# Performance work log

Measured on AMD Instinct MI355X. Metric: run time of the kernel, lower is better.

Reference implementation:

```python
import jax, jax.numpy as jnp
import numpy as np

B, T, DIM, H = 2, 2048, 512, 8
EPS = 1e-6


def setup_inputs() -> dict:
    key = jax.random.key(0)
    ks = jax.random.split(key, 6)
    scale = 0.05  # keep activations in a sane range for softmax/elu
    return {
        "x": jax.random.normal(ks[0], (B, T, DIM), dtype=jnp.float32),
        "Wq": jax.random.normal(ks[1], (DIM, DIM), dtype=jnp.float32) * scale,
        "Wk": jax.random.normal(ks[2], (DIM, DIM), dtype=jnp.float32) * scale,
        "Wv": jax.random.normal(ks[3], (DIM, DIM), dtype=jnp.float32) * scale,
        "Wo": jax.random.normal(ks[4], (DIM, DIM), dtype=jnp.float32) * scale,
        "bo": jax.random.normal(ks[5], (DIM,), dtype=jnp.float32) * scale,
    }


def reference(x, Wq, Wk, Wv, Wo, bo):
    b, t, dim = x.shape
    h = H
    d = dim // h
    # projections (nn.Linear: x @ W.T)
    q = x @ Wq.T
    k = x @ Wk.T
    v = x @ Wv.T
    mh = lambda z: z.reshape(b, t, h, d).transpose(0, 2, 1, 3)  # [b,h,t,d]
    q, k, v = mh(q), mh(k), mh(v)
    # causal linear attention with buckets = n (bucket size 1, no shift)
    q = jax.nn.softmax(q, axis=-1)
    k = jax.nn.elu(k) + 1.0  # psi
    k_cumsum = jnp.cumsum(k, axis=2)                       # [b,h,t,d]
    context = jnp.einsum('bhnd,bhne->bhnde', k, v)         # per-position outer products
    context = jnp.cumsum(context, axis=2)                  # causal prefix sum, [b,h,t,d,d]
    context = context / (k_cumsum[..., None] + EPS)        # safe_div
    attn = jnp.einsum('bhnd,bhnde->bhne', q, context)      # [b,h,t,d]
    out = attn.transpose(0, 2, 1, 3).reshape(b, t, dim)
    return out @ Wo.T + bo
```

## Files before the change

kernel.cpp:

```cpp
#include <hip/hip_runtime.h>

#define T_SEQ 2048
#define DIMM 512
#define NH 8
#define HD 64
#define BB 2
#define CHUNK 64
#define NCHUNK 32
#define EPSV 1e-6f
#define LDST 72
#define CST 132
#define PBUF 12288

typedef __attribute__((ext_vector_type(8))) short bf16x8;
typedef __attribute__((ext_vector_type(4))) short s16x4;
typedef __attribute__((ext_vector_type(4))) float f32x4;

static __device__ inline short f2bf(float f) {
    union { float f; unsigned u; } v; v.f = f;
    unsigned r = v.u + 0x7FFFu + ((v.u >> 16) & 1u);
    return (short)(r >> 16);
}
static __device__ inline float bf2f(short s) {
    union { unsigned u; float f; } v; v.u = ((unsigned)(unsigned short)s) << 16;
    return v.f;
}
static __device__ __forceinline__ void gload_lds16(const void* g, void* l) {
    __builtin_amdgcn_global_load_lds(
        (__attribute__((address_space(1))) void*)g,
        (__attribute__((address_space(3))) void*)l, 16, 0, 0);
}

__global__ __launch_bounds__(256) void convert_kernel(
    const float* __restrict__ x, const float* __restrict__ Wq,
    const float* __restrict__ Wk, const float* __restrict__ Wv,
    const float* __restrict__ Wo,
    short* __restrict__ xb, short* __restrict__ Wcat, short* __restrict__ Wob)
{
    const int u = blockIdx.x * 256 + threadIdx.x;
    const float* src; short* dst;
    if (u < 262144) {
        src = x + (size_t)u * 8; dst = xb + (size_t)u * 8;
    } else {
        const int v = u - 262144;
        const int o = (v & 32767) * 8;
        if (v < 32768)       { src = Wq + o; dst = Wcat + o; }
        else if (v < 65536)  { src = Wk + o; dst = Wcat + 262144 + o; }
        else if (v < 98304)  { src = Wv + o; dst = Wcat + 524288 + o; }
        else                 { src = Wo + o; dst = Wob + o; }
    }
    const float4 a = *(const float4*)src;
    const float4 b = *(const float4*)(src + 4);
    *(bf16x8*)dst = (bf16x8){f2bf(a.x), f2bf(a.y), f2bf(a.z), f2bf(a.w),
                             f2bf(b.x), f2bf(b.y), f2bf(b.z), f2bf(b.w)};
}

__global__ __launch_bounds__(256) void proj_mfma_kernel(
    const short* __restrict__ xb, const short* __restrict__ Wcat,
    short* __restrict__ Qs, short* __restrict__ Kbf,
    short* __restrict__ Ktb, short* __restrict__ Vt)
{
    __shared__ short S[2 * PBUF];
    short* Cs = S;
    const int m0 = blockIdx.x * 64;
    const int n0 = blockIdx.y * 128;
    const int which = blockIdx.y >> 2;
    const int tid = threadIdx.x;
    const int lane = tid & 63, w = tid >> 6;
    const int wr = w >> 1, wc = w & 1;
    const int fr = lane & 15, fg = lane >> 4;
    const int lrr = lane >> 3;
    const int sl8 = ((lane & 7) ^ lrr) * 8;
    const int xr = fr & 7;
    f32x4 acc[2][4] = {};

    #define STAGE(buf, k0)                                                       \
        {                                                                        \
            short* As_ = S + (buf) * PBUF;                                       \
            short* Bs_ = As_ + 4096;                                             \
            _Pragma("unroll")                                                    \
            for (int it = 0; it < 2; it++) {                                     \
                const int r0 = w * 16 + it * 8;                                  \
                gload_lds16(xb + (size_t)(m0 + r0 + lrr) * DIMM + (k0) + sl8,    \
                            &As_[r0 * 64]);                                      \
            }                                                                    \
            _Pragma("unroll")                                                    \
            for (int it = 0; it < 4; it++) {                                     \
                const int r0 = w * 32 + it * 8;                                  \
                gload_lds16(Wcat + (size_t)(n0 + r0 + lrr) * DIMM + (k0) + sl8,  \
                            &Bs_[r0 * 64]);                                      \
            }                                                                    \
        }

    STAGE(0, 0);
    STAGE(1, 64);

    #pragma unroll
    for (int t = 0; t < 8; t++) {
        if (t < 7) asm volatile("s_waitcnt vmcnt(6)" ::: "memory");
        else       asm volatile("s_waitcnt vmcnt(0)" ::: "memory");
        __builtin_amdgcn_sched_barrier(0);
        __builtin_amdgcn_s_barrier();
        __builtin_amdgcn_sched_barrier(0);
        {
            const short* As = S + (t & 1) * PBUF;
            const short* Bs = As + 4096;
            #pragma unroll
            for (int ks = 0; ks < 2; ks++) {
                const int cc = (((ks << 2) + fg) ^ xr) * 8;
                bf16x8 af[2], bfr[4];
                #pragma unroll
                for (int i = 0; i < 2; i++)
                    af[i] = *(const bf16x8*)&As[(wr * 32 + i * 16 + fr) * 64 + cc];
                #pragma unroll
                for (int j = 0; j < 4; j++)
                    bfr[j] = *(const bf16x8*)&Bs[(wc * 64 + j * 16 + fr) * 64 + cc];
                #pragma unroll
                for (int i = 0; i < 2; i++)
                    #pragma unroll
                    for (int j = 0; j < 4; j++)
                        acc[i][j] = __builtin_amdgcn_mfma_f32_16x16x32_bf16(af[i], bfr[j], acc[i][j], 0, 0, 0);
            }
        }
        __builtin_amdgcn_sched_barrier(0);
        __builtin_amdgcn_s_barrier();
        __builtin_amdgcn_sched_barrier(0);
        if (t < 6) STAGE(t & 1, (t + 2) * 64);
    }
    #undef STAGE

    #pragma unroll
    for (int i = 0; i < 2; i++)
        #pragma unroll
        for (int j = 0; j < 4; j++)
            #pragma unroll
            for (int reg = 0; reg < 4; reg++) {
                float val = acc[i][j][reg];
                if (which == 1) val = (val > 0.f) ? (val + 1.f) : __expf(val);
                Cs[(wr * 32 + i * 16 + fg * 4 + reg) * CST + wc * 64 + j * 16 + fr] = f2bf(val);
            }
    __syncthreads();

    const int b = m0 >> 11, t0 = m0 & (T_SEQ - 1);
    if (which == 0) {
        if (tid < 128) {
            const int r = tid & 63, hh = tid >> 6;
            const int head = (blockIdx.y & 3) * 2 + hh;
            s16x4 seg[16];
            #pragma unroll
            for (int s = 0; s < 16; s++) seg[s] = *(const s16x4*)&Cs[r * CST + hh * 64 + s * 4];
            float mx = -1e30f;
            #pragma unroll
            for (int s = 0; s < 16; s++)
                #pragma unroll
                for (int k = 0; k < 4; k++) mx = fmaxf(mx, bf2f(seg[s][k]));
            float sum = 0.f;
            #pragma unroll
            for (int s = 0; s < 16; s++)
                #pragma unroll
                for (int k = 0; k < 4; k++) sum += __expf(bf2f(seg[s][k]) - mx);
            const float inv = 1.f / sum;
            short* qp = Qs + (((size_t)(b * NH + head)) * T_SEQ + t0 + r) * HD;
            #pragma unroll
            for (int s = 0; s < 16; s += 2) {
                bf16x8 o;
                #pragma unroll
                for (int k = 0; k < 4; k++) o[k] = f2bf(__expf(bf2f(seg[s][k]) - mx) * inv);
                #pragma unroll
                for (int k = 0; k < 4; k++) o[4 + k] = f2bf(__expf(bf2f(seg[s + 1][k]) - mx) * inv);
                *(bf16x8*)(qp + s * 4) = o;
            }
        }
    } else if (which == 1) {
        if (tid < 128) {
            const int r = tid & 63, hh = tid >> 6;
            const int head = (blockIdx.y & 3) * 2 + hh;
            short* kp = Kbf + (((size_t)(b * NH + head)) * T_SEQ + t0 + r) * HD;
            #pragma unroll
            for (int s = 0; s < 8; s++) {
                const s16x4 a = *(const s16x4*)&Cs[r * CST + hh * 64 + s * 8];
                const s16x4 bq = *(const s16x4*)&Cs[r * CST + hh * 64 + s * 8 + 4];
                *(bf16x8*)(kp + s * 8) = (bf16x8){a[0], a[1], a[2], a[3], bq[0], bq[1], bq[2], bq[3]};
            }
        }
        {
            const int c = tid & 127, half = tid >> 7;
            const int head = (blockIdx.y & 3) * 2 + (c >> 6);
            const int d = c & 63;
            short* ktp = Ktb + (((size_t)(b * NH + head)) * HD + d) * T_SEQ + t0 + half * 32;
            #pragma unroll
            for (int s = 0; s < 4; s++) {
                bf16x8 o;
                #pragma unroll
                for (int k = 0; k < 8; k++) o[k] = Cs[(half * 32 + s * 8 + k) * CST + c];
                *(bf16x8*)(ktp + s * 8) = o;
            }
        }
    } else {
        const int c = tid & 127, half = tid >> 7;
        const int head = (blockIdx.y & 3) * 2 + (c >> 6);
        const int e = c & 63;
        short* vtp = Vt + (((size_t)(b * NH + head)) * HD + e) * T_SEQ + t0 + half * 32;
        #pragma unroll
        for (int s = 0; s < 4; s++) {
            bf16x8 o;
            #pragma unroll
            for (int k = 0; k < 8; k++) o[k] = Cs[(half * 32 + s * 8 + k) * CST + c];
            *(bf16x8*)(vtp + s * 8) = o;
        }
    }
}

__global__ __launch_bounds__(256) void chunk_sum_kernel(
    const short* __restrict__ Ktb, const short* __restrict__ Vt,
    float* __restrict__ Schunk, float* __restrict__ kchunk)
{
    __shared__ short VtL[64 * LDST];
    __shared__ short KtL[64 * LDST];
    __shared__ float ksp[4][64];
    const int bh = blockIdx.x >> 5, c = blockIdx.x & 31;
    const int tid = threadIdx.x;
    const int lane = tid & 63, w = tid >> 6;
    const int fr = lane & 15, fg = lane >> 4;
    #pragma unroll
    for (int it = 0; it < 2; it++) {
        const int qi = it * 256 + tid;
        const int r = qi >> 3, c8 = (qi & 7) * 8;
        *(bf16x8*)&VtL[r * LDST + c8] =
            *(const bf16x8*)(Vt + ((size_t)(bh * HD) + r) * T_SEQ + c * CHUNK + c8);
        *(bf16x8*)&KtL[r * LDST + c8] =
            *(const bf16x8*)(Ktb + ((size_t)(bh * HD) + r) * T_SEQ + c * CHUNK + c8);
    }
    __syncthreads();
    f32x4 acc[4] = {};
    #pragma unroll
    for (int ks = 0; ks < 2; ks++) {
        const bf16x8 av = *(const bf16x8*)&VtL[(w * 16 + fr) * LDST + ks * 32 + fg * 8];
        #pragma unroll
        for (int j = 0; j < 4; j++) {
            const bf16x8 bk = *(const bf16x8*)&KtL[(j * 16 + fr) * LDST + ks * 32 + fg * 8];
            acc[j] = __builtin_amdgcn_mfma_f32_16x16x32_bf16(av, bk, acc[j], 0, 0, 0);
        }
    }
    float* Sout = Schunk + ((size_t)bh * NCHUNK + c) * 4096;
    #pragma unroll
    for (int j = 0; j < 4; j++)
        #pragma unroll
        for (int reg = 0; reg < 4; reg++)
            Sout[(w * 16 + fg * 4 + reg) * 64 + j * 16 + fr] = acc[j][reg];
    float ps = 0.f;
    #pragma unroll
    for (int t = 0; t < 16; t++) ps += bf2f(KtL[lane * LDST + w * 16 + t]);
    ksp[w][lane] = ps;
    __syncthreads();
    if (tid < 64)
        kchunk[((size_t)bh * NCHUNK + c) * 64 + tid] =
            ksp[0][tid] + ksp[1][tid] + ksp[2][tid] + ksp[3][tid];
}

__global__ __launch_bounds__(256) void scan_kernel(float* __restrict__ Schunk,
                                                   float* __restrict__ kchunk)
{
    const int gid = blockIdx.x * 256 + threadIdx.x;
    if (blockIdx.x < 256) {
        const int bh = gid >> 12, i = gid & 4095;
        float run = 0.f;
        float* p = Schunk + (size_t)bh * NCHUNK * 4096 + i;
        for (int c = 0; c < NCHUNK; c++) { const float tv = p[c * 4096]; p[c * 4096] = run; run += tv; }
    } else {
        const int idx = gid - 65536;
        const int bh = idx >> 6, d = idx & 63;
        float run = 0.f;
        float* p = kchunk + (size_t)bh * NCHUNK * 64 + d;
        for (int c = 0; c < NCHUNK; c++) { const float tv = p[c * 64]; p[c * 64] = run; run += tv; }
    }
}

__global__ __launch_bounds__(256) void intra_kernel(
    const short* __restrict__ Qs, const short* __restrict__ Kbf,
    const short* __restrict__ Vt, const float* __restrict__ Schunk,
    const float* __restrict__ kchunk, short* __restrict__ attnb)
{
    __shared__ short B1[64 * LDST];
    __shared__ short B2[64 * LDST];
    __shared__ short KL[64 * LDST];
    __shared__ short VtL[64 * LDST];
    __shared__ short QnL[64 * LDST];
    __shared__ float gsum[4][64];
    __shared__ float kpre[64];
    const int bh = blockIdx.x >> 5, c = blockIdx.x & 31;
    const int tid = threadIdx.x;
    const int lane = tid & 63, w = tid >> 6;
    const int fr = lane & 15, fg = lane >> 4;
    const size_t tdbase = ((size_t)bh * T_SEQ + c * CHUNK) * HD;
    #pragma unroll
    for (int it = 0; it < 2; it++) {
        const int qi = it * 256 + tid;
        const int r = qi >> 3, c8 = (qi & 7) * 8;
        *(bf16x8*)&B1[r * LDST + c8]  = *(const bf16x8*)(Qs + tdbase + r * HD + c8);
        *(bf16x8*)&KL[r * LDST + c8]  = *(const bf16x8*)(Kbf + tdbase + r * HD + c8);
        *(bf16x8*)&VtL[r * LDST + c8] =
            *(const bf16x8*)(Vt + ((size_t)(bh * HD) + r) * T_SEQ + c * CHUNK + c8);
    }
    {
        const float* Sp = Schunk + ((size_t)bh * NCHUNK + c) * 4096;
        #pragma unroll
        for (int it = 0; it < 4; it++) {
            const int qi = it * 256 + tid;
            const int r = qi >> 4, c4 = (qi & 15) * 4;
            const float4 v = *(const float4*)(Sp + r * 64 + c4);
            *(s16x4*)&B2[r * LDST + c4] = (s16x4){f2bf(v.x), f2bf(v.y), f2bf(v.z), f2bf(v.w)};
        }
    }
    if (tid < 64) kpre[tid] = kchunk[((size_t)bh * NCHUNK + c) * 64 + tid];
    __syncthreads();
    {
        float s = 0.f;
        #pragma unroll
        for (int t = 0; t < 16; t++) s += bf2f(KL[(w * 16 + t) * LDST + lane]);
        gsum[w][lane] = s;
    }
    __syncthreads();
    {
        float run = kpre[lane];
        for (int gg = 0; gg < w; gg++) run += gsum[gg][lane];
        #pragma unroll
        for (int t0 = 0; t0 < 16; t0++) {
            const int t = w * 16 + t0;
            run += bf2f(KL[t * LDST + lane]);
            const float qv = bf2f(B1[t * LDST + lane]);
            QnL[t * LDST + lane] = f2bf(qv / (run + EPSV));
        }
    }
    __syncthreads();
    {
        f32x4 a1[4] = {};
        #pragma unroll
        for (int ks = 0; ks < 2; ks++) {
            const bf16x8 aq = *(const bf16x8*)&QnL[(w * 16 + fr) * LDST + ks * 32 + fg * 8];
            #pragma unroll
            for (int j = 0; j < 4; j++) {
                const bf16x8 bk = *(const bf16x8*)&KL[(j * 16 + fr) * LDST + ks * 32 + fg * 8];
                a1[j] = __builtin_amdgcn_mfma_f32_16x16x32_bf16(aq, bk, a1[j], 0, 0, 0);
            }
        }
        const int trow = w * 16 + fg * 4;
        #pragma unroll
        for (int j = 0; j < 4; j++)
            #pragma unroll
            for (int reg = 0; reg < 4; reg++) {
                const int t = trow + reg, s = j * 16 + fr;
                B1[t * LDST + s] = (s <= t) ? f2bf(a1[j][reg]) : (short)0;
            }
    }
    __syncthreads();
    {
        f32x4 a2[4] = {};
        #pragma unroll
        for (int ks = 0; ks < 2; ks++) {
            const bf16x8 aq = *(const bf16x8*)&QnL[(w * 16 + fr) * LDST + ks * 32 + fg * 8];
            const bf16x8 aa = *(const bf16x8*)&B1[(w * 16 + fr) * LDST + ks * 32 + fg * 8];
            #pragma unroll
            for (int j = 0; j < 4; j++) {
                const bf16x8 bs = *(const bf16x8*)&B2[(j * 16 + fr) * LDST + ks * 32 + fg * 8];
                const bf16x8 bv = *(const bf16x8*)&VtL[(j * 16 + fr) * LDST + ks * 32 + fg * 8];
                a2[j] = __builtin_amdgcn_mfma_f32_16x16x32_bf16(aq, bs, a2[j], 0, 0, 0);
                a2[j] = __builtin_amdgcn_mfma_f32_16x16x32_bf16(aa, bv, a2[j], 0, 0, 0);
            }
        }
        short* ap = attnb + tdbase;
        const int trow = w * 16 + fg * 4;
        #pragma unroll
        for (int j = 0; j < 4; j++)
            #pragma unroll
            for (int reg = 0; reg < 4; reg++)
                ap[(trow + reg) * HD + j * 16 + fr] = f2bf(a2[j][reg]);
    }
}

__global__ __launch_bounds__(256) void outproj_mfma_kernel(
    const short* __restrict__ attnb, const short* __restrict__ Wob,
    const float* __restrict__ bo, float* __restrict__ out)
{
    __shared__ short As[64 * 64];
    __shared__ short Bs[64 * 64];
    const int m0 = blockIdx.x * 64;
    const int n0 = blockIdx.y * 64;
    const int tid = threadIdx.x;
    const int lane = tid & 63, w = tid >> 6;
    const int fr = lane & 15, fg = lane >> 4;
    const int lr = lane >> 3, lc = (lane & 7) * 8;
    const int b = m0 >> 11, tbase = m0 & (T_SEQ - 1);
    f32x4 acc[4] = {};
    for (int k0 = 0; k0 < DIMM; k0 += 64) {
        const int h = k0 >> 6;
        #pragma unroll
        for (int it = 0; it < 2; it++) {
            const int r0 = w * 16 + it * 8;
            gload_lds16(attnb + (((size_t)(b * NH + h)) * T_SEQ + tbase + r0 + lr) * HD + lc,
                        &As[r0 * 64]);
            gload_lds16(Wob + (size_t)(n0 + r0 + lr) * DIMM + k0 + lc, &Bs[r0 * 64]);
        }
        __syncthreads();
        #pragma unroll
        for (int ks = 0; ks < 2; ks++) {
            const bf16x8 af = *(const bf16x8*)&As[(w * 16 + fr) * 64 + ks * 32 + fg * 8];
            #pragma unroll
            for (int j = 0; j < 4; j++) {
                const bf16x8 bfr = *(const bf16x8*)&Bs[(j * 16 + fr) * 64 + ks * 32 + fg * 8];
                acc[j] = __builtin_amdgcn_mfma_f32_16x16x32_bf16(af, bfr, acc[j], 0, 0, 0);
            }
        }
        __syncthreads();
    }
    #pragma unroll
    for (int j = 0; j < 4; j++)
        #pragma unroll
        for (int reg = 0; reg < 4; reg++) {
            const int m = m0 + w * 16 + fg * 4 + reg;
            const int n = n0 + j * 16 + fr;
            out[(size_t)m * DIMM + n] = acc[j][reg] + bo[n];
        }
}

extern "C" void kernel_launch(void* const* d_in, const int* in_sizes, int n_in,
                              void* d_out, int out_size, void* d_ws, size_t ws_size,
                              hipStream_t stream)
{
    const float* x  = (const float*)d_in[0];
    const float* Wq = (const float*)d_in[1];
    const float* Wk = (const float*)d_in[2];
    const float* Wv = (const float*)d_in[3];
    const float* Wo = (const float*)d_in[4];
    const float* bo = (const float*)d_in[5];
    float* out = (float*)d_out;

    const size_t NELEM = (size_t)BB * T_SEQ * DIMM;
    short* xb    = (short*)d_ws;
    short* Wcat  = xb + NELEM;
    short* Wob   = Wcat + 786432;
    short* Qs    = Wob + 262144;
    short* Kbf   = Qs + NELEM;
    short* Ktb   = Kbf + NELEM;
    short* Vt    = Ktb + NELEM;
    short* attnb = Vt + NELEM;
    float* Schunk = (float*)(attnb + NELEM);
    float* kchunk = Schunk + (size_t)BB * NH * NCHUNK * 4096;

    convert_kernel<<<dim3(1536), 256, 0, stream>>>(x, Wq, Wk, Wv, Wo, xb, Wcat, Wob);
    proj_mfma_kernel<<<dim3(64, 12), 256, 0, stream>>>(xb, Wcat, Qs, Kbf, Ktb, Vt);
    chunk_sum_kernel<<<dim3(BB * NH * NCHUNK), 256, 0, stream>>>(Ktb, Vt, Schunk, kchunk);
    scan_kernel<<<dim3(260), 256, 0, stream>>>(Schunk, kchunk);
    intra_kernel<<<dim3(BB * NH * NCHUNK), 256, 0, stream>>>(Qs, Kbf, Vt, Schunk, kchunk, attnb);
    outproj_mfma_kernel<<<dim3(64, 8), 256, 0, stream>>>(attnb, Wob, bo, out);
}
```

Baseline: 54.82 us.

## Widen projection GEMM tile to 64x256 per block with four heads

Measured after the change: 55.80 us. About the same (+1.8%).

```diff
diff --git a/kernel.cpp b/kernel.cpp
--- a/kernel.cpp
+++ b/kernel.cpp
@@ -9,8 +9,8 @@
 #define NCHUNK 32
 #define EPSV 1e-6f
 #define LDST 72
-#define CST 132
-#define PBUF 12288
+#define CSTW 258
+#define PB 20480
 
 typedef __attribute__((ext_vector_type(8))) short bf16x8;
 typedef __attribute__((ext_vector_type(4))) short s16x4;
@@ -60,23 +60,24 @@
     short* __restrict__ Qs, short* __restrict__ Kbf,
     short* __restrict__ Ktb, short* __restrict__ Vt)
 {
-    __shared__ short S[2 * PBUF];
+    extern __shared__ short S[];
     short* Cs = S;
     const int m0 = blockIdx.x * 64;
-    const int n0 = blockIdx.y * 128;
-    const int which = blockIdx.y >> 2;
+    const int n0 = blockIdx.y * 256;
+    const int which = blockIdx.y >> 1;
+    const int headbase = (blockIdx.y & 1) * 4;
     const int tid = threadIdx.x;
     const int lane = tid & 63, w = tid >> 6;
-    const int wr = w >> 1, wc = w & 1;
     const int fr = lane & 15, fg = lane >> 4;
     const int lrr = lane >> 3;
     const int sl8 = ((lane & 7) ^ lrr) * 8;
     const int xr = fr & 7;
-    f32x4 acc[2][4] = {};
+    const int b = m0 >> 11, t0 = m0 & (T_SEQ - 1);
+    f32x4 acc[4][4] = {};
 
     #define STAGE(buf, k0)                                                       \
         {                                                                        \
-            short* As_ = S + (buf) * PBUF;                                       \
+            short* As_ = S + (buf) * PB;                                         \
             short* Bs_ = As_ + 4096;                                             \
             _Pragma("unroll")                                                    \
             for (int it = 0; it < 2; it++) {                                     \
@@ -85,8 +86,8 @@
                             &As_[r0 * 64]);                                      \
             }                                                                    \
             _Pragma("unroll")                                                    \
-            for (int it = 0; it < 4; it++) {                                     \
-                const int r0 = w * 32 + it * 8;                                  \
+            for (int it = 0; it < 8; it++) {                                     \
+                const int r0 = w * 64 + it * 8;                                  \
                 gload_lds16(Wcat + (size_t)(n0 + r0 + lrr) * DIMM + (k0) + sl8,  \
                             &Bs_[r0 * 64]);                                      \
             }                                                                    \
@@ -97,29 +98,31 @@
 
     #pragma unroll
     for (int t = 0; t < 8; t++) {
-        if (t < 7) asm volatile("s_waitcnt vmcnt(6)" ::: "memory");
+        if (t < 7) asm volatile("s_waitcnt vmcnt(10)" ::: "memory");
         else       asm volatile("s_waitcnt vmcnt(0)" ::: "memory");
         __builtin_amdgcn_sched_barrier(0);
         __builtin_amdgcn_s_barrier();
         __builtin_amdgcn_sched_barrier(0);
         {
-            const short* As = S + (t & 1) * PBUF;
+            const short* As = S + (t & 1) * PB;
             const short* Bs = As + 4096;
             #pragma unroll
             for (int ks = 0; ks < 2; ks++) {
                 const int cc = (((ks << 2) + fg) ^ xr) * 8;
-                bf16x8 af[2], bfr[4];
+                bf16x8 af[4], bfr[4];
                 #pragma unroll
-                for (int i = 0; i < 2; i++)
-                    af[i] = *(const bf16x8*)&As[(wr * 32 + i * 16 + fr) * 64 + cc];
+                for (int i = 0; i < 4; i++)
+                    af[i] = *(const bf16x8*)&As[(i * 16 + fr) * 64 + cc];
                 #pragma unroll
                 for (int j = 0; j < 4; j++)
-                    bfr[j] = *(const bf16x8*)&Bs[(wc * 64 + j * 16 + fr) * 64 + cc];
+                    bfr[j] = *(const bf16x8*)&Bs[(w * 64 + j * 16 + fr) * 64 + cc];
+                __builtin_amdgcn_s_setprio(1);
                 #pragma unroll
-                for (int i = 0; i < 2; i++)
+                for (int i = 0; i < 4; i++)
                     #pragma unroll
                     for (int j = 0; j < 4; j++)
                         acc[i][j] = __builtin_amdgcn_mfma_f32_16x16x32_bf16(af[i], bfr[j], acc[i][j], 0, 0, 0);
+                __builtin_amdgcn_s_setprio(0);
             }
         }
         __builtin_amdgcn_sched_barrier(0);
@@ -130,82 +133,88 @@
     #undef STAGE
 
     #pragma unroll
-    for (int i = 0; i < 2; i++)
+    for (int i = 0; i < 4; i++)
         #pragma unroll
         for (int j = 0; j < 4; j++)
             #pragma unroll
             for (int reg = 0; reg < 4; reg++) {
                 float val = acc[i][j][reg];
                 if (which == 1) val = (val > 0.f) ? (val + 1.f) : __expf(val);
-                Cs[(wr * 32 + i * 16 + fg * 4 + reg) * CST + wc * 64 + j * 16 + fr] = f2bf(val);
-            }
-    __syncthreads();
-
-    const int b = m0 >> 11, t0 = m0 & (T_SEQ - 1);
+                Cs[(i * 16 + fg * 4 + reg) * CSTW + w * 64 + j * 16 + fr] = f2bf(val);
+            }
+    __syncthreads();
+
     if (which == 0) {
-        if (tid < 128) {
-            const int r = tid & 63, hh = tid >> 6;
-            const int head = (blockIdx.y & 3) * 2 + hh;
-            s16x4 seg[16];
-            #pragma unroll
-            for (int s = 0; s < 16; s++) seg[s] = *(const s16x4*)&Cs[r * CST + hh * 64 + s * 4];
-            float mx = -1e30f;
-            #pragma unroll
-            for (int s = 0; s < 16; s++)
-                #pragma unroll
-                for (int k = 0; k < 4; k++) mx = fmaxf(mx, bf2f(seg[s][k]));
-            float sum = 0.f;
-            #pragma unroll
-            for (int s = 0; s < 16; s++)
-                #pragma unroll
-                for (int k = 0; k < 4; k++) sum += __expf(bf2f(seg[s][k]) - mx);
-            const float inv = 1.f / sum;
-            short* qp = Qs + (((size_t)(b * NH + head)) * T_SEQ + t0 + r) * HD;
-            #pragma unroll
-            for (int s = 0; s < 16; s += 2) {
+        const int row = tid & 63, hl = tid >> 6;
+        const int head = headbase + hl;
+        const unsigned* cr = (const unsigned*)&Cs[row * CSTW + hl * 64];
+        unsigned u[32];
+        #pragma unroll
+        for (int s = 0; s < 32; s++) u[s] = cr[s];
+        float mx = -1e30f;
+        #pragma unroll
+        for (int s = 0; s < 32; s++) {
+            mx = fmaxf(mx, bf2f((short)(u[s] & 0xffff)));
+            mx = fmaxf(mx, bf2f((short)(u[s] >> 16)));
+        }
+        float sum = 0.f;
+        #pragma unroll
+        for (int s = 0; s < 32; s++) {
+            sum += __expf(bf2f((short)(u[s] & 0xffff)) - mx);
+            sum += __expf(bf2f((short)(u[s] >> 16)) - mx);
+        }
+        const float inv = 1.f / sum;
+        short* qp = Qs + (((size_t)(b * NH + head)) * T_SEQ + t0 + row) * HD;
+        #pragma unroll
+        for (int g = 0; g < 8; g++) {
+            bf16x8 o;
+            #pragma unroll
+            for (int k = 0; k < 4; k++) {
+                const unsigned uv = u[g * 4 + k];
+                o[2 * k]     = f2bf(__expf(bf2f((short)(uv & 0xffff)) - mx) * inv);
+                o[2 * k + 1] = f2bf(__expf(bf2f((short)(uv >> 16)) - mx) * inv);
+            }
+            *(bf16x8*)(qp + g * 8) = o;
+        }
+    } else if (which == 1) {
+        {
+            const int row = tid & 63, hl = tid >> 6;
+            const int head = headbase + hl;
+            const unsigned* cr = (const unsigned*)&Cs[row * CSTW + hl * 64];
+            short* kp = Kbf + (((size_t)(b * NH + head)) * T_SEQ + t0 + row) * HD;
+            #pragma unroll
+            for (int g = 0; g < 8; g++) {
                 bf16x8 o;
                 #pragma unroll
-                for (int k = 0; k < 4; k++) o[k] = f2bf(__expf(bf2f(seg[s][k]) - mx) * inv);
-                #pragma unroll
-                for (int k = 0; k < 4; k++) o[4 + k] = f2bf(__expf(bf2f(seg[s + 1][k]) - mx) * inv);
-                *(bf16x8*)(qp + s * 4) = o;
-            }
-        }
-    } else if (which == 1) {
-        if (tid < 128) {
-            const int r = tid & 63, hh = tid >> 6;
-            const int head = (blockIdx.y & 3) * 2 + hh;
-            short* kp = Kbf + (((size_t)(b * NH + head)) * T_SEQ + t0 + r) * HD;
+                for (int k = 0; k < 4; k++) {
+                    const unsigned uv = cr[g * 4 + k];
+                    o[2 * k]     = (short)(uv & 0xffff);
+                    o[2 * k + 1] = (short)(uv >> 16);
+                }
+                *(bf16x8*)(kp + g * 8) = o;
+            }
+        }
+        {
+            const int col = tid;
+            const int head = headbase + (col >> 6), d = col & 63;
+            short* ktp = Ktb + (((size_t)(b * NH + head)) * HD + d) * T_SEQ + t0;
             #pragma unroll
             for (int s = 0; s < 8; s++) {
-                const s16x4 a = *(const s16x4*)&Cs[r * CST + hh * 64 + s * 8];
-                const s16x4 bq = *(const s16x4*)&Cs[r * CST + hh * 64 + s * 8 + 4];
-                *(bf16x8*)(kp + s * 8) = (bf16x8){a[0], a[1], a[2], a[3], bq[0], bq[1], bq[2], bq[3]};
-            }
-        }
-        {
-            const int c = tid & 127, half = tid >> 7;
-            const int head = (blockIdx.y & 3) * 2 + (c >> 6);
-            const int d = c & 63;
-            short* ktp = Ktb + (((size_t)(b * NH + head)) * HD + d) * T_SEQ + t0 + half * 32;
-            #pragma unroll
-            for (int s = 0; s < 4; s++) {
                 bf16x8 o;
                 #pragma unroll
-                for (int k = 0; k < 8; k++) o[k] = Cs[(half * 32 + s * 8 + k) * CST + c];
+                for (int k = 0; k < 8; k++) o[k] = Cs[(s * 8 + k) * CSTW + col];
                 *(bf16x8*)(ktp + s * 8) = o;
             }
         }
     } else {
-        const int c = tid & 127, half = tid >> 7;
-        const int head = (blockIdx.y & 3) * 2 + (c >> 6);
-        const int e = c & 63;
-        short* vtp = Vt + (((size_t)(b * NH + head)) * HD + e) * T_SEQ + t0 + half * 32;
-        #pragma unroll
-        for (int s = 0; s < 4; s++) {
+        const int col = tid;
+        const int head = headbase + (col >> 6), e = col & 63;
+        short* vtp = Vt + (((size_t)(b * NH + head)) * HD + e) * T_SEQ + t0;
+        #pragma unroll
+        for (int s = 0; s < 8; s++) {
             bf16x8 o;
             #pragma unroll
-            for (int k = 0; k < 8; k++) o[k] = Cs[(half * 32 + s * 8 + k) * CST + c];
+            for (int k = 0; k < 8; k++) o[k] = Cs[(s * 8 + k) * CSTW + col];
             *(bf16x8*)(vtp + s * 8) = o;
         }
     }
@@ -447,8 +456,15 @@
     float* Schunk = (float*)(attnb + NELEM);
     float* kchunk = Schunk + (size_t)BB * NH * NCHUNK * 4096;
 
+    static bool attr_set = false;
+    if (!attr_set) {
+        hipFuncSetAttribute((const void*)proj_mfma_kernel,
+                            hipFuncAttributeMaxDynamicSharedMemorySize, 2 * PB * 2);
+        attr_set = true;
+    }
+
     convert_kernel<<<dim3(1536), 256, 0, stream>>>(x, Wq, Wk, Wv, Wo, xb, Wcat, Wob);
-    proj_mfma_kernel<<<dim3(64, 12), 256, 0, stream>>>(xb, Wcat, Qs, Kbf, Ktb, Vt);
+    proj_mfma_kernel<<<dim3(64, 6), 256, 2 * PB * 2, stream>>>(xb, Wcat, Qs, Kbf, Ktb, Vt);
     chunk_sum_kernel<<<dim3(BB * NH * NCHUNK), 256, 0, stream>>>(Ktb, Vt, Schunk, kchunk);
     scan_kernel<<<dim3(260), 256, 0, stream>>>(Schunk, kchunk);
     intra_kernel<<<dim3(BB * NH * NCHUNK), 256, 0, stream>>>(Qs, Kbf, Vt, Schunk, kchunk, attnb);
```

## Fold chunk-state prefix scan into intra kernel, drop separate scan launch

Applied to the files above, without the earlier changes.

Result: slower. 66.85 us (+21.9%).

```diff
diff --git a/kernel.cpp b/kernel.cpp
--- a/kernel.cpp
+++ b/kernel.cpp
@@ -258,24 +258,6 @@
             ksp[0][tid] + ksp[1][tid] + ksp[2][tid] + ksp[3][tid];
 }
 
-__global__ __launch_bounds__(256) void scan_kernel(float* __restrict__ Schunk,
-                                                   float* __restrict__ kchunk)
-{
-    const int gid = blockIdx.x * 256 + threadIdx.x;
-    if (blockIdx.x < 256) {
-        const int bh = gid >> 12, i = gid & 4095;
-        float run = 0.f;
-        float* p = Schunk + (size_t)bh * NCHUNK * 4096 + i;
-        for (int c = 0; c < NCHUNK; c++) { const float tv = p[c * 4096]; p[c * 4096] = run; run += tv; }
-    } else {
-        const int idx = gid - 65536;
-        const int bh = idx >> 6, d = idx & 63;
-        float run = 0.f;
-        float* p = kchunk + (size_t)bh * NCHUNK * 64 + d;
-        for (int c = 0; c < NCHUNK; c++) { const float tv = p[c * 64]; p[c * 64] = run; run += tv; }
-    }
-}
-
 __global__ __launch_bounds__(256) void intra_kernel(
     const short* __restrict__ Qs, const short* __restrict__ Kbf,
     const short* __restrict__ Vt, const float* __restrict__ Schunk,
@@ -303,16 +285,28 @@
             *(const bf16x8*)(Vt + ((size_t)(bh * HD) + r) * T_SEQ + c * CHUNK + c8);
     }
     {
-        const float* Sp = Schunk + ((size_t)bh * NCHUNK + c) * 4096;
-        #pragma unroll
-        for (int it = 0; it < 4; it++) {
-            const int qi = it * 256 + tid;
-            const int r = qi >> 4, c4 = (qi & 15) * 4;
-            const float4 v = *(const float4*)(Sp + r * 64 + c4);
-            *(s16x4*)&B2[r * LDST + c4] = (s16x4){f2bf(v.x), f2bf(v.y), f2bf(v.z), f2bf(v.w)};
-        }
-    }
-    if (tid < 64) kpre[tid] = kchunk[((size_t)bh * NCHUNK + c) * 64 + tid];
+        const float* Sbase = Schunk + ((size_t)bh * NCHUNK) * 4096 + tid * 16;
+        float accf[16] = {};
+        for (int cc = 0; cc < c; ++cc) {
+            #pragma unroll
+            for (int e = 0; e < 16; e += 4) {
+                const float4 v = *(const float4*)(Sbase + (size_t)cc * 4096 + e);
+                accf[e]     += v.x; accf[e + 1] += v.y;
+                accf[e + 2] += v.z; accf[e + 3] += v.w;
+            }
+        }
+        const int r = (tid * 16) >> 6, col0 = (tid * 16) & 63;
+        #pragma unroll
+        for (int e = 0; e < 16; e += 4)
+            *(s16x4*)&B2[r * LDST + col0 + e] =
+                (s16x4){f2bf(accf[e]), f2bf(accf[e + 1]), f2bf(accf[e + 2]), f2bf(accf[e + 3])};
+    }
+    if (tid < 64) {
+        float s = 0.f;
+        const float* kb = kchunk + (size_t)bh * NCHUNK * 64 + tid;
+        for (int cc = 0; cc < c; ++cc) s += kb[cc * 64];
+        kpre[tid] = s;
+    }
     __syncthreads();
     {
         float s = 0.f;
@@ -450,7 +444,6 @@
     convert_kernel<<<dim3(1536), 256, 0, stream>>>(x, Wq, Wk, Wv, Wo, xb, Wcat, Wob);
     proj_mfma_kernel<<<dim3(64, 12), 256, 0, stream>>>(xb, Wcat, Qs, Kbf, Ktb, Vt);
     chunk_sum_kernel<<<dim3(BB * NH * NCHUNK), 256, 0, stream>>>(Ktb, Vt, Schunk, kchunk);
-    scan_kernel<<<dim3(260), 256, 0, stream>>>(Schunk, kchunk);
     intra_kernel<<<dim3(BB * NH * NCHUNK), 256, 0, stream>>>(Qs, Kbf, Vt, Schunk, kchunk, attnb);
     outproj_mfma_kernel<<<dim3(64, 8), 256, 0, stream>>>(attnb, Wob, bo, out);
 }
```
